# Performance work log

Hardware: AMD Instinct MI355X
Metric: run time of the kernel (lower is better)

The kernel has to match this reference:

```python
import jax, jax.numpy as jnp
import numpy as np

N = 100   # num_nodes
D = 32    # num_dags
B = 8192  # batch_size
H = 32    # MLP hidden width


def setup_inputs() -> dict:
    key = jax.random.key(0)
    ks = jax.random.split(key, 6)
    x = jax.random.normal(ks[0], (B, N), dtype=jnp.float32)
    # binary adjacency masks for each sampled DAG
    A = (jax.random.uniform(ks[1], (D, N, N)) < 0.5).astype(jnp.float32)
    # per-dag topological order: a permutation of the N nodes
    order = jax.vmap(lambda k: jax.random.permutation(k, N))(
        jax.random.split(ks[2], D)).astype(jnp.int32)
    do_idx = 0  # intervened node
    # per-node MLP params: Linear(N+1, H) -> LeakyReLU -> Linear(H, 1)
    W1 = jax.random.normal(ks[3], (N, H, N + 1), dtype=jnp.float32) * (1.0 / np.sqrt(N + 1))
    b1 = jnp.zeros((N, H), dtype=jnp.float32)
    W2 = jax.random.normal(ks[4], (N, H), dtype=jnp.float32) * (1.0 / np.sqrt(H))
    b2 = jnp.zeros((N,), dtype=jnp.float32)
    return {"x": x, "A": A, "order": order, "do_idx": do_idx,
            "W1": W1, "b1": b1, "W2": W2, "b2": b2}


def reference(x, A, order, do_idx, W1, b1, W2, b2):
    Bn, Nn = x.shape
    # intervention: zero incoming edges of do_idx
    A = A.at[:, :, do_idx].set(0.0)

    def run_dag(A_d, order_d):
        def step(outputs, node):
            mask = A_d[:, node]                      # [N] parents of `node`
            ins = jnp.concatenate(
                [outputs * mask[None, :], x[:, node][:, None]], axis=1)  # [B, N+1]
            h = jax.nn.leaky_relu(ins @ W1[node].T + b1[node])           # [B, H]
            out = h @ W2[node] + b2[node]                                # [B]
            val = jnp.where(node == do_idx, x[:, node], out)
            return outputs.at[:, node].set(val), None

        outs, _ = jax.lax.scan(step, jnp.zeros((Bn, Nn), x.dtype), order_d)
        return outs  # [B, N]

    return jax.vmap(run_dag)(A, order)  # [D, B, N]
```

## Files before the change

kernel.cpp:

```cpp
#include <hip/hip_runtime.h>
#include <hip/hip_fp16.h>

#define NN 100
#define HH 32
#define BB 8192
#define DD 32
#define KP 128
#define TPB 1024

typedef _Float16 f16x8 __attribute__((ext_vector_type(8)));
typedef _Float16 f16x2 __attribute__((ext_vector_type(2)));
typedef __fp16 fph2 __attribute__((ext_vector_type(2)));
typedef float f32x4 __attribute__((ext_vector_type(4)));
typedef unsigned short ushort_t;
typedef unsigned int uint_t;
union FU { uint4 u; f16x8 h; };
union PU { fph2 p; f16x2 h; uint_t u; };

#define AS_GLOBAL __attribute__((address_space(1)))
#define AS_LDS    __attribute__((address_space(3)))

__global__ void prep_xth(const float* __restrict__ x, ushort_t* __restrict__ xTh) {
  int idx = blockIdx.x * 256 + threadIdx.x;
  if (idx >= BB * NN) return;
  int b = idx & (BB - 1);
  int n = idx >> 13;
  xTh[idx] = __half_as_ushort(__float2half_rn(x[(size_t)b * NN + n]));
}

__global__ void prep_w1m(const float* __restrict__ A, const float* __restrict__ W1,
                         const float* __restrict__ b1, ushort_t* __restrict__ W1M) {
  int idx = blockIdx.x * 256 + threadIdx.x;
  int tile = idx >> 12;
  int d = tile / NN;
  int node = tile - d * NN;
  int rem = idx & 4095;
  int j = rem >> 7;
  int k = rem & 127;
  float v = 0.f;
  if (k < NN) {
    float m = A[((size_t)d * NN + k) * NN + node];
    v = (m != 0.f) ? W1[((size_t)node * HH + j) * (NN + 1) + k] : 0.f;
  } else if (k == NN) {
    v = W1[((size_t)node * HH + j) * (NN + 1) + NN];
  } else if (k == NN + 1) {
    v = b1[node * HH + j];
  }
  int t = (j * KP + k) ^ ((j & 7) << 3);
  W1M[(size_t)tile * 4096 + t] = __half_as_ushort(__float2half_rn(v));
}

__global__ void prep_epi3(const float* __restrict__ W2, const float* __restrict__ b2,
                          uint_t* __restrict__ epi) {
  int idx = blockIdx.x * 256 + threadIdx.x;
  if (idx >= NN * 20) return;
  int node = idx / 20;
  int c = idx - node * 20;
  uint_t v = 0u;
  if (c < 16) {
    uint_t lo = __half_as_ushort(__float2half_rn(W2[node * HH + 2 * c]));
    uint_t hi = __half_as_ushort(__float2half_rn(W2[node * HH + 2 * c + 1]));
    v = lo | (hi << 16);
  } else if (c == 16) {
    v = __float_as_uint(b2[node]);
  }
  epi[idx] = v;
}

#define XS_OFF 65536
#define EPI_OFF 73728
#define SMEM_BYTES (73728 + 8000)

__global__ __launch_bounds__(TPB, 8) void dag_mfma_ss(
    const ushort_t* __restrict__ xTh,
    const int* __restrict__ order,
    const int* __restrict__ do_idx_p,
    const ushort_t* __restrict__ W1M,
    const uint_t* __restrict__ epi_g,
    float* __restrict__ out)
{
  __shared__ __align__(16) char smem[SMEM_BYTES];
  ushort_t* stage = (ushort_t*)smem;
  const char* sp = (const char*)smem;
  uint_t* epi_l = (uint_t*)(smem + EPI_OFF);

  const int d = blockIdx.y;
  const int bx = blockIdx.x;
  const int tid = threadIdx.x;
  const int w = tid >> 6;
  const int lane = tid & 63;
  const int g = lane >> 4;
  const int n16 = lane & 15;
  const int di = __builtin_amdgcn_readfirstlane(do_idx_p[0]);

  {
    const uint4* s4 = (const uint4*)epi_g;
    uint4* d4 = (uint4*)epi_l;
    for (int i = tid; i < 500; i += TPB) d4[i] = s4[i];
  }

  const ushort_t* Wd = W1M + (size_t)d * NN * 4096;
  const int* ord = order + d * NN;

  int vs[4];
#pragma unroll
  for (int S = 0; S < 4; ++S) {
    int hw = n16 * 128 + ((8 * g) ^ ((n16 & 3) << 3)) + 32 * (S ^ ((n16 >> 2) & 1));
    vs[S] = 2 * hw + 32768;
  }
  int xso = XS_OFF + (w * 32 + n16) * 2 + 4096;

  int nd[4], nn[4];
#pragma unroll
  for (int q = 0; q < 4; ++q) nd[q] = __builtin_amdgcn_readfirstlane(ord[q]);
  if (w < 8) {
#pragma unroll
    for (int q = 0; q < 4; ++q) {
      const ushort_t* gsrc = Wd + (size_t)nd[q] * 4096 + tid * 8;
      __builtin_amdgcn_global_load_lds((const AS_GLOBAL void*)gsrc,
          (AS_LDS void*)(stage + q * 4096 + (w << 9)), 16, 0, 0);
    }
  }
#pragma unroll
  for (int q = 0; q < 4; ++q) {
    if (w == q) {
      const ushort_t* gx = xTh + (size_t)nd[q] * BB + bx * 512 + lane * 8;
      __builtin_amdgcn_global_load_lds((const AS_GLOBAL void*)gx,
          (AS_LDS void*)(smem + XS_OFF + q * 1024), 16, 0, 0);
    }
  }

  uint4 breg[2][4];
#pragma unroll
  for (int nt = 0; nt < 2; ++nt) {
#pragma unroll
    for (int S = 0; S < 4; ++S) breg[nt][S] = make_uint4(0u, 0u, 0u, 0u);
    breg[nt][3].z = (g == 0) ? 0x3C000000u : 0u;
  }

  const f32x4 zero4 = {0.f, 0.f, 0.f, 0.f};
  PU c001; c001.u = 0x211F211Fu;

#pragma unroll 1
  for (int ss = 0; ss < 25; ++ss) {
    asm volatile("s_waitcnt vmcnt(0) lgkmcnt(0)" ::: "memory");
    __builtin_amdgcn_s_barrier();
    __builtin_amdgcn_sched_barrier(0);

#pragma unroll
    for (int S = 0; S < 4; ++S) vs[S] ^= 32768;
    xso ^= 4096;

    const bool more = (ss < 24);
    if (more) {
#pragma unroll
      for (int q = 0; q < 4; ++q)
        nn[q] = __builtin_amdgcn_readfirstlane(ord[4 * (ss + 1) + q]);
      const int dsts = (((ss + 1) & 1) << 14);
      if (w < 8) {
#pragma unroll
        for (int q = 0; q < 4; ++q) {
          const ushort_t* gsrc = Wd + (size_t)nn[q] * 4096 + tid * 8;
          __builtin_amdgcn_global_load_lds((const AS_GLOBAL void*)gsrc,
              (AS_LDS void*)(stage + dsts + q * 4096 + (w << 9)), 16, 0, 0);
        }
      }
      const int xdst = XS_OFF + (((ss + 1) & 1) << 12);
#pragma unroll
      for (int q = 0; q < 4; ++q) {
        if (w == q) {
          const ushort_t* gx = xTh + (size_t)nn[q] * BB + bx * 512 + lane * 8;
          __builtin_amdgcn_global_load_lds((const AS_GLOBAL void*)gx,
              (AS_LDS void*)(smem + xdst + q * 1024), 16, 0, 0);
        }
      }
    }

#pragma unroll
    for (int q = 0; q < 4; ++q) {
      const int node = nd[q];

      ushort_t xb[2];
#pragma unroll
      for (int nt = 0; nt < 2; ++nt)
        xb[nt] = *(const ushort_t*)(sp + xso + q * 1024 + nt * 32);

#pragma unroll
      for (int nt = 0; nt < 2; ++nt) {
        uint_t ins = 0x3C000000u | (uint_t)xb[nt];
        breg[nt][3].z = (g == 0) ? ins : breg[nt][3].z;
      }

      float val[2];
      if (node != di) {
        const char* ep = (const char*)epi_l + node * 80;
        const float b2n = *(const float*)(ep + 64);

        f32x4 acc[2];
        float p0[2];

        {
          __builtin_amdgcn_s_setprio(1);
#pragma unroll
          for (int S = 0; S < 4; ++S) {
            FU a0;
            a0.u = *(const uint4*)(sp + vs[S] + q * 8192);
#pragma unroll
            for (int nt = 0; nt < 2; ++nt) {
              FU bu; bu.u = breg[nt][S];
              if (S == 0)
                acc[nt] = __builtin_amdgcn_mfma_f32_16x16x32_f16(a0.h, bu.h, zero4, 0, 0, 0);
              else
                acc[nt] = __builtin_amdgcn_mfma_f32_16x16x32_f16(a0.h, bu.h, acc[nt], 0, 0, 0);
            }
          }
          __builtin_amdgcn_s_setprio(0);
          const uint2 wlo = *(const uint2*)(ep + 8 * g);
          PU w01, w23; w01.u = wlo.x; w23.u = wlo.y;
#pragma unroll
          for (int nt = 0; nt < 2; ++nt) {
            PU h01, h23;
            h01.p = __builtin_amdgcn_cvt_pkrtz(acc[nt][0], acc[nt][1]);
            h23.p = __builtin_amdgcn_cvt_pkrtz(acc[nt][2], acc[nt][3]);
            h01.p = __builtin_elementwise_max(h01.p, h01.p * c001.p);
            h23.p = __builtin_elementwise_max(h23.p, h23.p * c001.p);
            float p = __builtin_amdgcn_fdot2(h01.h, w01.h, 0.f, false);
            p0[nt] = __builtin_amdgcn_fdot2(h23.h, w23.h, p, false);
          }
        }

        {
          __builtin_amdgcn_s_setprio(1);
#pragma unroll
          for (int S = 0; S < 4; ++S) {
            FU a1;
            a1.u = *(const uint4*)(sp + vs[S] + q * 8192 + 4096);
#pragma unroll
            for (int nt = 0; nt < 2; ++nt) {
              FU bu; bu.u = breg[nt][S];
              if (S == 0)
                acc[nt] = __builtin_amdgcn_mfma_f32_16x16x32_f16(a1.h, bu.h, zero4, 0, 0, 0);
              else
                acc[nt] = __builtin_amdgcn_mfma_f32_16x16x32_f16(a1.h, bu.h, acc[nt], 0, 0, 0);
            }
          }
          __builtin_amdgcn_s_setprio(0);
          const uint2 whi = *(const uint2*)(ep + 32 + 8 * g);
          PU w45, w67; w45.u = whi.x; w67.u = whi.y;
#pragma unroll
          for (int nt = 0; nt < 2; ++nt) {
            PU h45, h67;
            h45.p = __builtin_amdgcn_cvt_pkrtz(acc[nt][0], acc[nt][1]);
            h67.p = __builtin_amdgcn_cvt_pkrtz(acc[nt][2], acc[nt][3]);
            h45.p = __builtin_elementwise_max(h45.p, h45.p * c001.p);
            h67.p = __builtin_elementwise_max(h67.p, h67.p * c001.p);
            float p = __builtin_amdgcn_fdot2(h45.h, w45.h, p0[nt], false);
            p = __builtin_amdgcn_fdot2(h67.h, w67.h, p, false);
            p += __shfl_xor(p, 16, 64);
            p += __shfl_xor(p, 32, 64);
            val[nt] = p + b2n;
          }
        }
      } else {
#pragma unroll
        for (int nt = 0; nt < 2; ++nt)
          val[nt] = __half2float(__ushort_as_half(xb[nt]));
      }

      const int sn = node >> 5;
      const int en2 = (node >> 1) & 3;
      const int gn = (node >> 3) & 3;
      const int hin = node & 1;
      const bool own = (g == gn);
      ushort_t hv[2];
#pragma unroll
      for (int nt = 0; nt < 2; ++nt) hv[nt] = __half_as_ushort(__float2half_rn(val[nt]));
#pragma unroll
      for (int S = 0; S < 4; ++S) {
        if (S != sn) continue;
#pragma unroll
        for (int nt = 0; nt < 2; ++nt) {
          uint4& Bq = breg[nt][S];
          uint_t hvn = (uint_t)hv[nt];
          if (en2 == 0) {
            uint_t old = Bq.x;
            uint_t nw = hin ? ((old & 0x0000FFFFu) | (hvn << 16)) : ((old & 0xFFFF0000u) | hvn);
            Bq.x = own ? nw : old;
          } else if (en2 == 1) {
            uint_t old = Bq.y;
            uint_t nw = hin ? ((old & 0x0000FFFFu) | (hvn << 16)) : ((old & 0xFFFF0000u) | hvn);
            Bq.y = own ? nw : old;
          } else if (en2 == 2) {
            uint_t old = Bq.z;
            uint_t nw = hin ? ((old & 0x0000FFFFu) | (hvn << 16)) : ((old & 0xFFFF0000u) | hvn);
            Bq.z = own ? nw : old;
          } else {
            uint_t old = Bq.w;
            uint_t nw = hin ? ((old & 0x0000FFFFu) | (hvn << 16)) : ((old & 0xFFFF0000u) | hvn);
            Bq.w = own ? nw : old;
          }
        }
      }
    }

#pragma unroll
    for (int q = 0; q < 4; ++q) nd[q] = nn[q];
  }

  ushort_t* tbuf = (ushort_t*)smem;
#pragma unroll 1
  for (int c = 0; c < 16; ++c) {
    __syncthreads();
    if (w == c) {
#pragma unroll
      for (int nt = 0; nt < 2; ++nt) {
        int r = nt * 16 + n16;
#pragma unroll
        for (int S = 0; S < 4; ++S) {
          int k = 32 * S + 8 * g;
          *(uint2*)&tbuf[r * 132 + k] = make_uint2(breg[nt][S].x, breg[nt][S].y);
          *(uint2*)&tbuf[r * 132 + k + 4] = make_uint2(breg[nt][S].z, breg[nt][S].w);
        }
      }
    }
    __syncthreads();
    const size_t obase = ((size_t)d * BB + bx * 512 + c * 32) * NN;
    for (int idx = tid; idx < 32 * NN; idx += TPB) {
      int rl = idx / NN;
      int col = idx - rl * NN;
      out[obase + idx] = __half2float(__ushort_as_half(tbuf[rl * 132 + col]));
    }
  }
}

extern "C" void kernel_launch(void* const* d_in, const int* in_sizes, int n_in,
                              void* d_out, int out_size, void* d_ws, size_t ws_size,
                              hipStream_t stream) {
  const float* x     = (const float*)d_in[0];
  const float* A     = (const float*)d_in[1];
  const int* order   = (const int*)d_in[2];
  const int* do_idx  = (const int*)d_in[3];
  const float* W1    = (const float*)d_in[4];
  const float* b1    = (const float*)d_in[5];
  const float* W2    = (const float*)d_in[6];
  const float* b2    = (const float*)d_in[7];
  float* out = (float*)d_out;

  char* ws = (char*)d_ws;
  const size_t XTH_B = (size_t)BB * NN * 2;
  const size_t W1M_B = (size_t)DD * NN * 4096 * 2;
  ushort_t* xTh = (ushort_t*)ws;
  ushort_t* W1M = (ushort_t*)(ws + XTH_B);
  uint_t* epi   = (uint_t*)(ws + XTH_B + W1M_B);

  hipLaunchKernelGGL(prep_xth, dim3((BB * NN) / 256), dim3(256), 0, stream, x, xTh);
  hipLaunchKernelGGL(prep_w1m, dim3((DD * NN * 4096) / 256), dim3(256), 0, stream,
                     A, W1, b1, W1M);
  hipLaunchKernelGGL(prep_epi3, dim3((NN * 20 + 255) / 256), dim3(256), 0, stream,
                     W2, b2, epi);
  hipLaunchKernelGGL(dag_mfma_ss, dim3(BB / 512, DD), dim3(TPB), 0, stream,
                     xTh, order, do_idx, W1M, epi, out);
}
```

Baseline: 265.6 us.

## Reindex parents by topological slot to skip empty MFMA K-chunks

Weight tiles are re-laid out so the K dimension is indexed by topological position of the parent rather than node id. A node at step t can only depend on earlier slots, so only the first (t+34)/32 K-chunks are loaded and multiplied. The cost this targets is the MFMA work and weight-tile loads for the zero-masked future parents. To support this, the kernel adds an inverse permutation table in LDS for the output scatter, a permuted x layout so each lane reads both batch values with one 32-bit load, and a repacked W2 epilogue read as one uint4. In exchange it adds per-step branching on the chunk count and extra indirection in the prep and output phases.

```diff
diff --git a/kernel.cpp b/kernel.cpp
--- a/kernel.cpp
+++ b/kernel.cpp
@@ -5,7 +5,6 @@
 #define HH 32
 #define BB 8192
 #define DD 32
-#define KP 128
 #define TPB 1024
 
 typedef _Float16 f16x8 __attribute__((ext_vector_type(8)));
@@ -25,64 +24,79 @@
   if (idx >= BB * NN) return;
   int b = idx & (BB - 1);
   int n = idx >> 13;
-  xTh[idx] = __half_as_ushort(__float2half_rn(x[(size_t)b * NN + n]));
+  int chunk = b >> 9;
+  int r = b & 511;
+  int wv = r >> 5, i = r & 31;
+  int pp = wv * 32 + ((i & 15) << 1) + (i >> 4);
+  xTh[(size_t)n * BB + chunk * 512 + pp] =
+      __half_as_ushort(__float2half_rn(x[(size_t)b * NN + n]));
 }
 
-__global__ void prep_w1m(const float* __restrict__ A, const float* __restrict__ W1,
-                         const float* __restrict__ b1, ushort_t* __restrict__ W1M) {
+__global__ void prep_w1p(const float* __restrict__ A, const float* __restrict__ W1,
+                         const float* __restrict__ b1, const int* __restrict__ order,
+                         ushort_t* __restrict__ W1P) {
   int idx = blockIdx.x * 256 + threadIdx.x;
   int tile = idx >> 12;
   int d = tile / NN;
   int node = tile - d * NN;
-  int rem = idx & 4095;
-  int j = rem >> 7;
-  int k = rem & 127;
+  int p = idx & 4095;
+  int s = p >> 10;
+  int j = (p >> 5) & 31;
+  int w5 = p & 31;
+  int o_sw = w5 >> 3;
+  int e = w5 & 7;
+  int kk = ((o_sw ^ (j & 3)) << 3) | e;
+  int slot = (s << 5) | kk;
   float v = 0.f;
-  if (k < NN) {
-    float m = A[((size_t)d * NN + k) * NN + node];
-    v = (m != 0.f) ? W1[((size_t)node * HH + j) * (NN + 1) + k] : 0.f;
-  } else if (k == NN) {
+  if (slot == 0) {
+    v = b1[node * HH + j];
+  } else if (slot == 1) {
     v = W1[((size_t)node * HH + j) * (NN + 1) + NN];
-  } else if (k == NN + 1) {
-    v = b1[node * HH + j];
-  }
-  int t = (j * KP + k) ^ ((j & 7) << 3);
-  W1M[(size_t)tile * 4096 + t] = __half_as_ushort(__float2half_rn(v));
+  } else {
+    int pos = slot - 2;
+    if (pos < NN) {
+      int parent = order[d * NN + pos];
+      float m = A[((size_t)d * NN + parent) * NN + node];
+      v = (m != 0.f) ? W1[((size_t)node * HH + j) * (NN + 1) + parent] : 0.f;
+    }
+  }
+  W1P[idx] = __half_as_ushort(__float2half_rn(v));
 }
 
-__global__ void prep_epi3(const float* __restrict__ W2, const float* __restrict__ b2,
-                          uint_t* __restrict__ epi) {
+__global__ void prep_epi4(const float* __restrict__ W2, const float* __restrict__ b2,
+                          uint_t* __restrict__ epi4, float* __restrict__ b2t) {
   int idx = blockIdx.x * 256 + threadIdx.x;
-  if (idx >= NN * 20) return;
-  int node = idx / 20;
-  int c = idx - node * 20;
-  uint_t v = 0u;
-  if (c < 16) {
-    uint_t lo = __half_as_ushort(__float2half_rn(W2[node * HH + 2 * c]));
-    uint_t hi = __half_as_ushort(__float2half_rn(W2[node * HH + 2 * c + 1]));
-    v = lo | (hi << 16);
-  } else if (c == 16) {
-    v = __float_as_uint(b2[node]);
-  }
-  epi[idx] = v;
+  if (idx < NN * 16) {
+    int node = idx >> 4;
+    int g = (idx >> 2) & 3;
+    int r = idx & 3;
+    int j0 = ((r & 2) << 3) + 4 * g + ((r & 1) << 1);
+    uint_t lo = __half_as_ushort(__float2half_rn(W2[node * HH + j0]));
+    uint_t hi = __half_as_ushort(__float2half_rn(W2[node * HH + j0 + 1]));
+    epi4[idx] = lo | (hi << 16);
+  } else if (idx < NN * 16 + NN) {
+    int node = idx - NN * 16;
+    b2t[node] = b2[node];
+  }
 }
 
 #define XS_OFF 65536
-#define EPI_OFF 73728
-#define SMEM_BYTES (73728 + 8000)
-
-__global__ __launch_bounds__(TPB, 8) void dag_mfma_ss(
+#define EPI4_OFF 73728
+#define B2T_OFF 80128
+#define INV_OFF 80528
+#define SMEM_BYTES 80736
+
+__global__ __launch_bounds__(TPB, 8) void dag_mfma_ks(
     const ushort_t* __restrict__ xTh,
     const int* __restrict__ order,
     const int* __restrict__ do_idx_p,
-    const ushort_t* __restrict__ W1M,
-    const uint_t* __restrict__ epi_g,
+    const ushort_t* __restrict__ W1P,
+    const uint_t* __restrict__ epi4_g,
+    const float* __restrict__ b2t_g,
     float* __restrict__ out)
 {
   __shared__ __align__(16) char smem[SMEM_BYTES];
-  ushort_t* stage = (ushort_t*)smem;
   const char* sp = (const char*)smem;
-  uint_t* epi_l = (uint_t*)(smem + EPI_OFF);
 
   const int d = blockIdx.y;
   const int bx = blockIdx.x;
@@ -92,33 +106,34 @@
   const int g = lane >> 4;
   const int n16 = lane & 15;
   const int di = __builtin_amdgcn_readfirstlane(do_idx_p[0]);
+  const int* ord = order + d * NN;
 
   {
-    const uint4* s4 = (const uint4*)epi_g;
-    uint4* d4 = (uint4*)epi_l;
-    for (int i = tid; i < 500; i += TPB) d4[i] = s4[i];
-  }
-
-  const ushort_t* Wd = W1M + (size_t)d * NN * 4096;
-  const int* ord = order + d * NN;
-
-  int vs[4];
-#pragma unroll
-  for (int S = 0; S < 4; ++S) {
-    int hw = n16 * 128 + ((8 * g) ^ ((n16 & 3) << 3)) + 32 * (S ^ ((n16 >> 2) & 1));
-    vs[S] = 2 * hw + 32768;
-  }
-  int xso = XS_OFF + (w * 32 + n16) * 2 + 4096;
-
-  int nd[4], nn[4];
-#pragma unroll
-  for (int q = 0; q < 4; ++q) nd[q] = __builtin_amdgcn_readfirstlane(ord[q]);
-  if (w < 8) {
-#pragma unroll
-    for (int q = 0; q < 4; ++q) {
-      const ushort_t* gsrc = Wd + (size_t)nd[q] * 4096 + tid * 8;
-      __builtin_amdgcn_global_load_lds((const AS_GLOBAL void*)gsrc,
-          (AS_LDS void*)(stage + q * 4096 + (w << 9)), 16, 0, 0);
+    const uint4* s4 = (const uint4*)epi4_g;
+    uint4* d4 = (uint4*)(smem + EPI4_OFF);
+    for (int i = tid; i < 400; i += TPB) d4[i] = s4[i];
+    if (tid < NN) {
+      ((float*)(smem + B2T_OFF))[tid] = b2t_g[tid];
+      ((ushort_t*)(smem + INV_OFF))[ord[tid]] = (ushort_t)(tid + 2);
+    }
+  }
+
+  const ushort_t* Wd = W1P + (size_t)d * NN * 4096;
+
+  const int vsw = n16 * 64 + ((g ^ (n16 & 3)) << 4);
+  int tsb = 32768;
+  int xtb = 4096;
+
+  int nd[4], nn2[4];
+#pragma unroll
+  for (int q = 0; q < 4; ++q) { nd[q] = __builtin_amdgcn_readfirstlane(ord[q]); nn2[q] = nd[q]; }
+  {
+    const int q = w >> 2, c = w & 3;
+    const char* gb = (const char*)Wd + (size_t)nd[q] * 8192;
+    if (c < 2) {
+      __builtin_amdgcn_global_load_lds(
+          (const AS_GLOBAL void*)(gb + c * 1024 + (size_t)lane * 16),
+          (AS_LDS void*)(smem + q * 8192 + c * 1024), 16, 0, 0);
     }
   }
 #pragma unroll
@@ -135,7 +150,7 @@
   for (int nt = 0; nt < 2; ++nt) {
 #pragma unroll
     for (int S = 0; S < 4; ++S) breg[nt][S] = make_uint4(0u, 0u, 0u, 0u);
-    breg[nt][3].z = (g == 0) ? 0x3C000000u : 0u;
+    breg[nt][0].x = (g == 0) ? 0x00003C00u : 0u;
   }
 
   const f32x4 zero4 = {0.f, 0.f, 0.f, 0.f};
@@ -147,76 +162,93 @@
     __builtin_amdgcn_s_barrier();
     __builtin_amdgcn_sched_barrier(0);
 
-#pragma unroll
-    for (int S = 0; S < 4; ++S) vs[S] ^= 32768;
-    xso ^= 4096;
+    tsb ^= 32768;
+    xtb ^= 4096;
 
     const bool more = (ss < 24);
     if (more) {
 #pragma unroll
       for (int q = 0; q < 4; ++q)
-        nn[q] = __builtin_amdgcn_readfirstlane(ord[4 * (ss + 1) + q]);
-      const int dsts = (((ss + 1) & 1) << 14);
-      if (w < 8) {
-#pragma unroll
-        for (int q = 0; q < 4; ++q) {
-          const ushort_t* gsrc = Wd + (size_t)nn[q] * 4096 + tid * 8;
-          __builtin_amdgcn_global_load_lds((const AS_GLOBAL void*)gsrc,
-              (AS_LDS void*)(stage + dsts + q * 4096 + (w << 9)), 16, 0, 0);
+        nn2[q] = __builtin_amdgcn_readfirstlane(ord[4 * (ss + 1) + q]);
+      const int dset = tsb ^ 32768;
+      {
+        const int q = w >> 2, c = w & 3;
+        const int t_n = 4 * (ss + 1) + q;
+        const int nS2 = ((t_n + 34) >> 5) << 1;
+        const char* gb = (const char*)Wd + (size_t)nn2[q] * 8192;
+        char* lb = (char*)smem + dset + q * 8192;
+        if (c < nS2) {
+          __builtin_amdgcn_global_load_lds(
+              (const AS_GLOBAL void*)(gb + c * 1024 + (size_t)lane * 16),
+              (AS_LDS void*)(lb + c * 1024), 16, 0, 0);
+        }
+        if (c + 4 < nS2) {
+          __builtin_amdgcn_global_load_lds(
+              (const AS_GLOBAL void*)(gb + (c + 4) * 1024 + (size_t)lane * 16),
+              (AS_LDS void*)(lb + (c + 4) * 1024), 16, 0, 0);
         }
       }
-      const int xdst = XS_OFF + (((ss + 1) & 1) << 12);
+      const int xd = XS_OFF + (xtb ^ 4096);
 #pragma unroll
       for (int q = 0; q < 4; ++q) {
         if (w == q) {
-          const ushort_t* gx = xTh + (size_t)nn[q] * BB + bx * 512 + lane * 8;
+          const ushort_t* gx = xTh + (size_t)nn2[q] * BB + bx * 512 + lane * 8;
           __builtin_amdgcn_global_load_lds((const AS_GLOBAL void*)gx,
-              (AS_LDS void*)(smem + xdst + q * 1024), 16, 0, 0);
+              (AS_LDS void*)(smem + xd + q * 1024), 16, 0, 0);
         }
       }
     }
 
 #pragma unroll
     for (int q = 0; q < 4; ++q) {
+      const int t = 4 * ss + q;
+      const int st = t + 2;
+      const int nS = (t + 34) >> 5;
       const int node = nd[q];
 
-      ushort_t xb[2];
-#pragma unroll
-      for (int nt = 0; nt < 2; ++nt)
-        xb[nt] = *(const ushort_t*)(sp + xso + q * 1024 + nt * 32);
-
-#pragma unroll
-      for (int nt = 0; nt < 2; ++nt) {
-        uint_t ins = 0x3C000000u | (uint_t)xb[nt];
-        breg[nt][3].z = (g == 0) ? ins : breg[nt][3].z;
-      }
+      const uint_t xw = *(const uint_t*)(sp + XS_OFF + xtb + w * 64 + n16 * 4 + q * 1024);
+
+      breg[0][0].x = (g == 0) ? (0x00003C00u | (xw << 16)) : breg[0][0].x;
+      breg[1][0].x = (g == 0) ? (0x00003C00u | (xw & 0xFFFF0000u)) : breg[1][0].x;
 
       float val[2];
       if (node != di) {
-        const char* ep = (const char*)epi_l + node * 80;
-        const float b2n = *(const float*)(ep + 64);
+        const uint4 w4 = *(const uint4*)(sp + EPI4_OFF + node * 64 + g * 16);
+        const float b2n = *(const float*)(sp + B2T_OFF + node * 4);
 
         f32x4 acc[2];
         float p0[2];
-
+        const int tb = tsb + q * 8192;
+
+        __builtin_amdgcn_s_setprio(1);
         {
-          __builtin_amdgcn_s_setprio(1);
-#pragma unroll
-          for (int S = 0; S < 4; ++S) {
-            FU a0;
-            a0.u = *(const uint4*)(sp + vs[S] + q * 8192);
-#pragma unroll
-            for (int nt = 0; nt < 2; ++nt) {
-              FU bu; bu.u = breg[nt][S];
-              if (S == 0)
-                acc[nt] = __builtin_amdgcn_mfma_f32_16x16x32_f16(a0.h, bu.h, zero4, 0, 0, 0);
-              else
-                acc[nt] = __builtin_amdgcn_mfma_f32_16x16x32_f16(a0.h, bu.h, acc[nt], 0, 0, 0);
-            }
-          }
-          __builtin_amdgcn_s_setprio(0);
-          const uint2 wlo = *(const uint2*)(ep + 8 * g);
-          PU w01, w23; w01.u = wlo.x; w23.u = wlo.y;
+          FU a, b0, b1_;
+          a.u = *(const uint4*)(sp + tb + vsw);
+          b0.u = breg[0][0]; b1_.u = breg[1][0];
+          acc[0] = __builtin_amdgcn_mfma_f32_16x16x32_f16(a.h, b0.h, zero4, 0, 0, 0);
+          acc[1] = __builtin_amdgcn_mfma_f32_16x16x32_f16(a.h, b1_.h, zero4, 0, 0, 0);
+          if (nS > 1) {
+            a.u = *(const uint4*)(sp + tb + 2048 + vsw);
+            b0.u = breg[0][1]; b1_.u = breg[1][1];
+            acc[0] = __builtin_amdgcn_mfma_f32_16x16x32_f16(a.h, b0.h, acc[0], 0, 0, 0);
+            acc[1] = __builtin_amdgcn_mfma_f32_16x16x32_f16(a.h, b1_.h, acc[1], 0, 0, 0);
+          }
+          if (nS > 2) {
+            a.u = *(const uint4*)(sp + tb + 4096 + vsw);
+            b0.u = breg[0][2]; b1_.u = breg[1][2];
+            acc[0] = __builtin_amdgcn_mfma_f32_16x16x32_f16(a.h, b0.h, acc[0], 0, 0, 0);
+            acc[1] = __builtin_amdgcn_mfma_f32_16x16x32_f16(a.h, b1_.h, acc[1], 0, 0, 0);
+          }
+          if (nS > 3) {
+            a.u = *(const uint4*)(sp + tb + 6144 + vsw);
+            b0.u = breg[0][3]; b1_.u = breg[1][3];
+            acc[0] = __builtin_amdgcn_mfma_f32_16x16x32_f16(a.h, b0.h, acc[0], 0, 0, 0);
+            acc[1] = __builtin_amdgcn_mfma_f32_16x16x32_f16(a.h, b1_.h, acc[1], 0, 0, 0);
+          }
+        }
+        __builtin_amdgcn_s_setprio(0);
+        {
+          PU w01, w23; w01.u = w4.x; w23.u = w4.y;
 #pragma unroll
           for (int nt = 0; nt < 2; ++nt) {
             PU h01, h23;
@@ -229,24 +261,35 @@
           }
         }
 
+        __builtin_amdgcn_s_setprio(1);
         {
-          __builtin_amdgcn_s_setprio(1);
-#pragma unroll
-          for (int S = 0; S < 4; ++S) {
-            FU a1;
-            a1.u = *(const uint4*)(sp + vs[S] + q * 8192 + 4096);
-#pragma unroll
-            for (int nt = 0; nt < 2; ++nt) {
-              FU bu; bu.u = breg[nt][S];
-              if (S == 0)
-                acc[nt] = __builtin_amdgcn_mfma_f32_16x16x32_f16(a1.h, bu.h, zero4, 0, 0, 0);
-              else
-                acc[nt] = __builtin_amdgcn_mfma_f32_16x16x32_f16(a1.h, bu.h, acc[nt], 0, 0, 0);
-            }
-          }
-          __builtin_amdgcn_s_setprio(0);
-          const uint2 whi = *(const uint2*)(ep + 32 + 8 * g);
-          PU w45, w67; w45.u = whi.x; w67.u = whi.y;
+          FU a, b0, b1_;
+          a.u = *(const uint4*)(sp + tb + 1024 + vsw);
+          b0.u = breg[0][0]; b1_.u = breg[1][0];
+          acc[0] = __builtin_amdgcn_mfma_f32_16x16x32_f16(a.h, b0.h, zero4, 0, 0, 0);
+          acc[1] = __builtin_amdgcn_mfma_f32_16x16x32_f16(a.h, b1_.h, zero4, 0, 0, 0);
+          if (nS > 1) {
+            a.u = *(const uint4*)(sp + tb + 3072 + vsw);
+            b0.u = breg[0][1]; b1_.u = breg[1][1];
+            acc[0] = __builtin_amdgcn_mfma_f32_16x16x32_f16(a.h, b0.h, acc[0], 0, 0, 0);
+            acc[1] = __builtin_amdgcn_mfma_f32_16x16x32_f16(a.h, b1_.h, acc[1], 0, 0, 0);
+          }
+          if (nS > 2) {
+            a.u = *(const uint4*)(sp + tb + 5120 + vsw);
+            b0.u = breg[0][2]; b1_.u = breg[1][2];
+            acc[0] = __builtin_amdgcn_mfma_f32_16x16x32_f16(a.h, b0.h, acc[0], 0, 0, 0);
+            acc[1] = __builtin_amdgcn_mfma_f32_16x16x32_f16(a.h, b1_.h, acc[1], 0, 0, 0);
+          }
+          if (nS > 3) {
+            a.u = *(const uint4*)(sp + tb + 7168 + vsw);
+            b0.u = breg[0][3]; b1_.u = breg[1][3];
+            acc[0] = __builtin_amdgcn_mfma_f32_16x16x32_f16(a.h, b0.h, acc[0], 0, 0, 0);
+            acc[1] = __builtin_amdgcn_mfma_f32_16x16x32_f16(a.h, b1_.h, acc[1], 0, 0, 0);
+          }
+        }
+        __builtin_amdgcn_s_setprio(0);
+        {
+          PU w45, w67; w45.u = w4.z; w67.u = w4.w;
 #pragma unroll
           for (int nt = 0; nt < 2; ++nt) {
             PU h45, h67;
@@ -262,19 +305,18 @@
           }
         }
       } else {
-#pragma unroll
-        for (int nt = 0; nt < 2; ++nt)
-          val[nt] = __half2float(__ushort_as_half(xb[nt]));
+        val[0] = __half2float(__ushort_as_half((ushort_t)(xw & 0xFFFFu)));
+        val[1] = __half2float(__ushort_as_half((ushort_t)(xw >> 16)));
       }
 
-      const int sn = node >> 5;
-      const int en2 = (node >> 1) & 3;
-      const int gn = (node >> 3) & 3;
-      const int hin = node & 1;
+      const int sn = st >> 5;
+      const int en2 = (st >> 1) & 3;
+      const int gn = (st >> 3) & 3;
+      const int hin = st & 1;
       const bool own = (g == gn);
       ushort_t hv[2];
-#pragma unroll
-      for (int nt = 0; nt < 2; ++nt) hv[nt] = __half_as_ushort(__float2half_rn(val[nt]));
+      hv[0] = __half_as_ushort(__float2half_rn(val[0]));
+      hv[1] = __half_as_ushort(__float2half_rn(val[1]));
 #pragma unroll
       for (int S = 0; S < 4; ++S) {
         if (S != sn) continue;
@@ -304,10 +346,11 @@
     }
 
 #pragma unroll
-    for (int q = 0; q < 4; ++q) nd[q] = nn[q];
+    for (int q = 0; q < 4; ++q) nd[q] = nn2[q];
   }
 
   ushort_t* tbuf = (ushort_t*)smem;
+  const ushort_t* invp = (const ushort_t*)(smem + INV_OFF);
 #pragma unroll 1
   for (int c = 0; c < 16; ++c) {
     __syncthreads();
@@ -328,7 +371,8 @@
     for (int idx = tid; idx < 32 * NN; idx += TPB) {
       int rl = idx / NN;
       int col = idx - rl * NN;
-      out[obase + idx] = __half2float(__ushort_as_half(tbuf[rl * 132 + col]));
+      int slot = invp[col];
+      out[obase + idx] = __half2float(__ushort_as_half(tbuf[rl * 132 + slot]));
     }
   }
 }
@@ -348,16 +392,17 @@
 
   char* ws = (char*)d_ws;
   const size_t XTH_B = (size_t)BB * NN * 2;
-  const size_t W1M_B = (size_t)DD * NN * 4096 * 2;
-  ushort_t* xTh = (ushort_t*)ws;
-  ushort_t* W1M = (ushort_t*)(ws + XTH_B);
-  uint_t* epi   = (uint_t*)(ws + XTH_B + W1M_B);
+  const size_t W1P_B = (size_t)DD * NN * 4096 * 2;
+  ushort_t* xTh  = (ushort_t*)ws;
+  ushort_t* W1P  = (ushort_t*)(ws + XTH_B);
+  uint_t* epi4   = (uint_t*)(ws + XTH_B + W1P_B);
+  float* b2t     = (float*)(ws + XTH_B + W1P_B + 6400);
 
   hipLaunchKernelGGL(prep_xth, dim3((BB * NN) / 256), dim3(256), 0, stream, x, xTh);
-  hipLaunchKernelGGL(prep_w1m, dim3((DD * NN * 4096) / 256), dim3(256), 0, stream,
-                     A, W1, b1, W1M);
-  hipLaunchKernelGGL(prep_epi3, dim3((NN * 20 + 255) / 256), dim3(256), 0, stream,
-                     W2, b2, epi);
-  hipLaunchKernelGGL(dag_mfma_ss, dim3(BB / 512, DD), dim3(TPB), 0, stream,
-                     xTh, order, do_idx, W1M, epi, out);
+  hipLaunchKernelGGL(prep_w1p, dim3((DD * NN * 4096) / 256), dim3(256), 0, stream,
+                     A, W1, b1, order, W1P);
+  hipLaunchKernelGGL(prep_epi4, dim3((NN * 16 + NN + 255) / 256), dim3(256), 0, stream,
+                     W2, b2, epi4, b2t);
+  hipLaunchKernelGGL(dag_mfma_ks, dim3(BB / 512, DD), dim3(TPB), 0, stream,
+                     xTh, order, do_idx, W1P, epi4, b2t, out);
 }
```

New measurement: 522.3 us. 1.97x slower.
